# Optimization experiments

Hardware: AMD Instinct MI355X
Metric: run time of the kernel (lower is better)

## Reference

```python
import jax, jax.numpy as jnp
import numpy as np

N, E, IN, OUT, R, B = 20000, 640000, 256, 800, 8, 8


def setup_inputs() -> dict:
    key = jax.random.key(0)
    k0, k1, k2, k3, k4, k5 = jax.random.split(key, 6)
    x = jax.random.normal(k0, (N, IN), dtype=jnp.float32)
    edge_index = jax.random.randint(k1, (2, E), 0, N, dtype=jnp.int32)
    edge_type = jax.random.randint(k2, (E,), 0, R, dtype=jnp.int32)
    # basis-decomposed relation weights: W_r = sum_b att[r,b] * bases[b]
    bases = jax.random.normal(k3, (B, IN, OUT), dtype=jnp.float32) * 0.05
    att = jax.random.normal(k4, (R, B), dtype=jnp.float32) * 0.3
    root = jax.random.normal(k5, (IN, OUT), dtype=jnp.float32) * 0.05
    bias = jnp.zeros((OUT,), dtype=jnp.float32)
    return {"x": x, "edge_index": edge_index, "edge_type": edge_type,
            "bases": bases, "att": att, "root": root, "bias": bias}


def reference(x, edge_index, edge_type, bases, att, root, bias):
    # RGCNConv (basis decomposition, scatter-add aggregation):
    #   out[v] = sum_{(u->v, r) in edges} x[u] @ W_r  +  x[v] @ root  +  bias
    # Efficient form: first segment-sum x[src] per (dst, relation), then one
    # dense contraction with the R relation weights (math-identical for add-aggr).
    n, in_dim = x.shape
    r, b = att.shape
    W = jnp.einsum('rb,bio->rio', att, bases)          # [R, IN, OUT]
    src, dst = edge_index[0], edge_index[1]
    seg = dst.astype(jnp.int32) * r + edge_type.astype(jnp.int32)
    # per-(node, relation) sums of source features: [N*R, IN] -> [N, R, IN]
    s = jax.ops.segment_sum(x[src], seg, num_segments=n * r).reshape(n, r, in_dim)
    out = jnp.einsum('nri,rio->no', s, W) + x @ root + bias
    return out
```

## Files before the change

### kernel.cpp

```cpp
#include <hip/hip_runtime.h>


#define N_NODES 20000
#define N_EDGES 640000
#define IN_DIM  256
#define OUT_DIM 800
#define NREL    8
#define NSEG    160000
#define KS      2048
#define KTOT    2304
#define NPAD    1024
#define NB      625

#define BM 256
#define BN 160
#define BK 64
#define NKT (KTOT / BK)
#define MT  79
#define NT  5
#define NWG (MT * NT)
#define ABYTES 32768
#define LBUF 53248

#define XCAST_B (N_NODES * 64 / 256)
#define WCAT_B  ((KTOT / 8) * 4)
#define INIT_NWG (NB + XCAST_B + WCAT_B)

typedef float f32x4_t __attribute__((ext_vector_type(4)));
typedef short short8_t __attribute__((ext_vector_type(8)));

__device__ __forceinline__ unsigned short f2bf(float f) {
  unsigned u = __float_as_uint(f);
  u += 0x7fffu + ((u >> 16) & 1u);
  return (unsigned short)(u >> 16);
}

__device__ __forceinline__ float bflo(unsigned w) { return __uint_as_float(w << 16); }
__device__ __forceinline__ float bfhi(unsigned w) { return __uint_as_float(w & 0xffff0000u); }

__device__ __forceinline__ void gload16(const void* g, void* l) {
  __builtin_amdgcn_global_load_lds(
      (const __attribute__((address_space(1))) void*)g,
      (__attribute__((address_space(3))) void*)l, 16, 0, 0);
}

__global__ void init_kernel(const float* __restrict__ x,
                            const float* __restrict__ bases,
                            const float* __restrict__ att,
                            const float* __restrict__ root,
                            int* __restrict__ cnt,
                            unsigned short* __restrict__ abf,
                            unsigned short* __restrict__ wcatT) {
  const int b = blockIdx.x;
  const int t = threadIdx.x;
  if (b < NB) {
    cnt[b * 256 + t] = 0;
  } else if (b < NB + XCAST_B) {
    const int id = (b - NB) * 256 + t;
    const int row = id >> 6, lane = id & 63;
    const float4 v = ((const float4*)x)[(size_t)row * 64 + lane];
    union { unsigned short u[4]; uint2 q; } pk;
    pk.u[0] = f2bf(v.x); pk.u[1] = f2bf(v.y);
    pk.u[2] = f2bf(v.z); pk.u[3] = f2bf(v.w);
    *(uint2*)(abf + (size_t)row * KTOT + KS + lane * 4) = pk.q;
  } else {
    const int rem = b - NB - XCAST_B;
    const int kc = rem >> 2, ng = rem & 3;
    const int k0 = kc * 8;
    const int n  = ng * 256 + t;
    if (n >= OUT_DIM) return;
    union { unsigned short u[8]; uint4 q; } pk;
    if (k0 < KS) {
      const int r = k0 >> 8, i0 = k0 & 255;
      float av[8];
      #pragma unroll
      for (int bb = 0; bb < 8; ++bb) av[bb] = att[r * 8 + bb];
      #pragma unroll
      for (int j = 0; j < 8; ++j) {
        float v = 0.f;
        #pragma unroll
        for (int bb = 0; bb < 8; ++bb)
          v += av[bb] * bases[((size_t)bb * IN_DIM + i0 + j) * OUT_DIM + n];
        pk.u[j] = f2bf(v);
      }
    } else {
      #pragma unroll
      for (int j = 0; j < 8; ++j)
        pk.u[j] = f2bf(root[(size_t)(k0 - KS + j) * OUT_DIM + n]);
    }
    *(uint4*)(wcatT + (size_t)n * KTOT + k0) = pk.q;
  }
}


__global__ void hist_kernel(const int* __restrict__ ei, const int* __restrict__ et,
                            int* __restrict__ cnt) {
  const int e = blockIdx.x * 256 + threadIdx.x;
  const int seg = ei[N_EDGES + e] * NREL + et[e];
  atomicAdd(&cnt[seg], 1);
}

__global__ void scan_reduce_kernel(const int* __restrict__ cnt, int* __restrict__ bsum) {
  __shared__ int sm[256];
  const int t = threadIdx.x;
  sm[t] = cnt[blockIdx.x * 256 + t];
  __syncthreads();
  for (int s = 128; s > 0; s >>= 1) {
    if (t < s) sm[t] += sm[t + s];
    __syncthreads();
  }
  if (t == 0) bsum[blockIdx.x] = sm[0];
}

__global__ void scan_bsum_kernel(int* __restrict__ bsum) {
  __shared__ int sm[1024];
  const int t = threadIdx.x;
  const int v = (t < NB) ? bsum[t] : 0;
  sm[t] = v;
  __syncthreads();
  for (int s = 1; s < 1024; s <<= 1) {
    const int a = (t >= s) ? sm[t - s] : 0;
    __syncthreads();
    sm[t] += a;
    __syncthreads();
  }
  if (t < NB) bsum[t] = sm[t] - v;
}

__global__ void scan_final_kernel(const int* __restrict__ cnt, const int* __restrict__ bsum,
                                  int* __restrict__ off, int* __restrict__ cur) {
  __shared__ int sm[256];
  const int t = threadIdx.x;
  const int g = blockIdx.x * 256 + t;
  const int v = cnt[g];
  sm[t] = v;
  __syncthreads();
  for (int s = 1; s < 256; s <<= 1) {
    const int a = (t >= s) ? sm[t - s] : 0;
    __syncthreads();
    sm[t] += a;
    __syncthreads();
  }
  const int ex = sm[t] - v + bsum[blockIdx.x];
  off[g] = ex;
  cur[g] = ex;
}

__global__ void reorder_kernel(const int* __restrict__ ei, const int* __restrict__ et,
                               int* __restrict__ cur, int* __restrict__ sorted_src) {
  const int e = blockIdx.x * 256 + threadIdx.x;
  const int seg = ei[N_EDGES + e] * NREL + et[e];
  const int pos = atomicAdd(&cur[seg], 1);
  sorted_src[pos] = ei[e];
}

__global__ void aggregate_kernel(const int* __restrict__ cnt, const int* __restrict__ off,
                                 const int* __restrict__ sorted_src,
                                 unsigned short* __restrict__ abf) {
  const int seg = __builtin_amdgcn_readfirstlane(blockIdx.x * 4 + (threadIdx.x >> 6));
  const int l = threadIdx.x & 63;
  const int half = l >> 5;
  const int sl = l & 31;
  const int ne = cnt[seg];
  const int o  = off[seg];
  float a0 = 0.f, a1 = 0.f, a2 = 0.f, a3 = 0.f;
  float a4 = 0.f, a5 = 0.f, a6 = 0.f, a7 = 0.f;
  int j = 0;
  for (; j + 2 <= ne; j += 2) {
    const int s = sorted_src[o + j + half];
    const uint4 u = *(const uint4*)(abf + (size_t)s * KTOT + KS + sl * 8);
    a0 += bflo(u.x); a1 += bfhi(u.x); a2 += bflo(u.y); a3 += bfhi(u.y);
    a4 += bflo(u.z); a5 += bfhi(u.z); a6 += bflo(u.w); a7 += bfhi(u.w);
  }
  if (j < ne && half == 0) {
    const int s = sorted_src[o + j];
    const uint4 u = *(const uint4*)(abf + (size_t)s * KTOT + KS + sl * 8);
    a0 += bflo(u.x); a1 += bfhi(u.x); a2 += bflo(u.y); a3 += bfhi(u.y);
    a4 += bflo(u.z); a5 += bfhi(u.z); a6 += bflo(u.w); a7 += bfhi(u.w);
  }
  a0 += __shfl_xor(a0, 32); a1 += __shfl_xor(a1, 32);
  a2 += __shfl_xor(a2, 32); a3 += __shfl_xor(a3, 32);
  a4 += __shfl_xor(a4, 32); a5 += __shfl_xor(a5, 32);
  a6 += __shfl_xor(a6, 32); a7 += __shfl_xor(a7, 32);
  if (half == 0) {
    const int node = seg >> 3, r = seg & 7;
    union { unsigned short u[8]; uint4 q; } pk;
    pk.u[0] = f2bf(a0); pk.u[1] = f2bf(a1); pk.u[2] = f2bf(a2); pk.u[3] = f2bf(a3);
    pk.u[4] = f2bf(a4); pk.u[5] = f2bf(a5); pk.u[6] = f2bf(a6); pk.u[7] = f2bf(a7);
    *(uint4*)(abf + (size_t)node * KTOT + r * IN_DIM + sl * 8) = pk.q;
  }
}

__global__ __launch_bounds__(512) void gemm_kernel(
    const unsigned short* __restrict__ abf,
    const unsigned short* __restrict__ wcatT,
    const float* __restrict__ bias, float* __restrict__ out) {
  __shared__ __align__(16) char lds[3 * LBUF];

  const int lin = blockIdx.x;
  const int q8 = NWG >> 3, r8 = NWG & 7;
  const int xcd = lin & 7, idx = lin >> 3;
  const int wg = (xcd < r8 ? xcd * (q8 + 1) : r8 * (q8 + 1) + (xcd - r8) * q8) + idx;
  const int row0 = (wg / NT) * BM;
  const int col0 = (wg % NT) * BN;

  const int tid = threadIdx.x;
  const int w = tid >> 6, l = tid & 63;
  const int wm = w >> 1, wn = w & 1;
  const int la = l & 15, lg = l >> 4;
  const int l3 = l >> 3;
  const int sch = (l & 7) ^ l3;

  const unsigned short* gA[4];
  #pragma unroll
  for (int i = 0; i < 4; ++i) {
    int ga = row0 + i * 64 + w * 8 + l3;
    ga = (ga < N_NODES) ? ga : (N_NODES - 1);
    gA[i] = abf + (size_t)ga * KTOT + sch * 8;
  }
  const int b2row = (w < 4) ? (128 + w * 8 + l3) : ((w - 4) * 8 + l3);
  const unsigned short* gB0 = wcatT + (size_t)(col0 + w * 8 + l3) * KTOT + sch * 8;
  const unsigned short* gB1 = wcatT + (size_t)(col0 + 64 + w * 8 + l3) * KTOT + sch * 8;
  const unsigned short* gB2 = wcatT + (size_t)(col0 + b2row) * KTOT + sch * 8;
  const int dB2 = (w < 4) ? (ABYTES + 16384 + w * 1024) : (ABYTES + (w - 4) * 1024);

  f32x4_t acc[4][5];
  #pragma unroll
  for (int i = 0; i < 4; ++i)
    #pragma unroll
    for (int j = 0; j < 5; ++j)
      acc[i][j] = (f32x4_t)(0.0f);

  auto stage_all = [&](int buf, int kt) {
    char* base = lds + buf * LBUF;
    const int ko = kt * BK;
    gload16(gA[0] + ko, base + w * 1024);
    gload16(gA[1] + ko, base + 8192 + w * 1024);
    gload16(gA[2] + ko, base + 16384 + w * 1024);
    gload16(gA[3] + ko, base + 24576 + w * 1024);
    gload16(gB0 + ko, base + ABYTES + w * 1024);
    gload16(gB1 + ko, base + ABYTES + 8192 + w * 1024);
    gload16(gB2 + ko, base + dB2);
  };

  stage_all(0, 0);
  stage_all(1, 1);

  for (int kt = 0; kt < NKT; ++kt) {
    const int cbuf = kt % 3;
    const int pbuf = (kt + 2) % 3;
    const bool pf = (kt + 2) < NKT;
    const int pko = (kt + 2) * BK;
    const char* Ab = lds + cbuf * LBUF;
    const char* Bb = Ab + ABYTES;
    char* pbase = lds + pbuf * LBUF;

    if (kt + 1 < NKT) { asm volatile("s_waitcnt vmcnt(7)" ::: "memory"); }
    else              { asm volatile("s_waitcnt vmcnt(0)" ::: "memory"); }
    __builtin_amdgcn_sched_barrier(0);
    __builtin_amdgcn_s_barrier();

    short8_t af0, af1, bfv[5];

    {
      const int r0 = wm * 64 + la, r1 = wm * 64 + 16 + la;
      af0 = *(const short8_t*)(Ab + r0 * 128 + ((lg << 4) ^ ((r0 & 7) << 4)));
      af1 = *(const short8_t*)(Ab + r1 * 128 + ((lg << 4) ^ ((r1 & 7) << 4)));
      #pragma unroll
      for (int nf = 0; nf < 5; ++nf) {
        const int rr = wn * 80 + nf * 16 + la;
        bfv[nf] = *(const short8_t*)(Bb + rr * 128 + ((lg << 4) ^ ((rr & 7) << 4)));
      }
      if (pf) { gload16(gA[0] + pko, pbase + w * 1024);
                gload16(gA[1] + pko, pbase + 8192 + w * 1024); }
      __builtin_amdgcn_s_barrier();
      asm volatile("s_waitcnt lgkmcnt(0)" ::: "memory");
      __builtin_amdgcn_sched_barrier(0);
      __builtin_amdgcn_s_setprio(1);
      #pragma unroll
      for (int nf = 0; nf < 5; ++nf)
        acc[0][nf] = __builtin_amdgcn_mfma_f32_16x16x32_bf16(af0, bfv[nf], acc[0][nf], 0, 0, 0);
      #pragma unroll
      for (int nf = 0; nf < 5; ++nf)
        acc[1][nf] = __builtin_amdgcn_mfma_f32_16x16x32_bf16(af1, bfv[nf], acc[1][nf], 0, 0, 0);
      __builtin_amdgcn_s_setprio(0);
      __builtin_amdgcn_s_barrier();
    }
    {
      const int r0 = wm * 64 + 32 + la, r1 = wm * 64 + 48 + la;
      af0 = *(const short8_t*)(Ab + r0 * 128 + ((lg << 4) ^ ((r0 & 7) << 4)));
      af1 = *(const short8_t*)(Ab + r1 * 128 + ((lg << 4) ^ ((r1 & 7) << 4)));
      if (pf) { gload16(gA[2] + pko, pbase + 16384 + w * 1024);
                gload16(gA[3] + pko, pbase + 24576 + w * 1024); }
      __builtin_amdgcn_s_barrier();
      asm volatile("s_waitcnt lgkmcnt(0)" ::: "memory");
      __builtin_amdgcn_sched_barrier(0);
      __builtin_amdgcn_s_setprio(1);
      #pragma unroll
      for (int nf = 0; nf < 5; ++nf)
        acc[2][nf] = __builtin_amdgcn_mfma_f32_16x16x32_bf16(af0, bfv[nf], acc[2][nf], 0, 0, 0);
      #pragma unroll
      for (int nf = 0; nf < 5; ++nf)
        acc[3][nf] = __builtin_amdgcn_mfma_f32_16x16x32_bf16(af1, bfv[nf], acc[3][nf], 0, 0, 0);
      __builtin_amdgcn_s_setprio(0);
      __builtin_amdgcn_s_barrier();
    }
    {
      const int r0 = wm * 64 + la, r1 = wm * 64 + 16 + la;
      af0 = *(const short8_t*)(Ab + r0 * 128 + (((4 + lg) << 4) ^ ((r0 & 7) << 4)));
      af1 = *(const short8_t*)(Ab + r1 * 128 + (((4 + lg) << 4) ^ ((r1 & 7) << 4)));
      #pragma unroll
      for (int nf = 0; nf < 5; ++nf) {
        const int rr = wn * 80 + nf * 16 + la;
        bfv[nf] = *(const short8_t*)(Bb + rr * 128 + (((4 + lg) << 4) ^ ((rr & 7) << 4)));
      }
      if (pf) { gload16(gB0 + pko, pbase + ABYTES + w * 1024);
                gload16(gB1 + pko, pbase + ABYTES + 8192 + w * 1024); }
      __builtin_amdgcn_s_barrier();
      asm volatile("s_waitcnt lgkmcnt(0)" ::: "memory");
      __builtin_amdgcn_sched_barrier(0);
      __builtin_amdgcn_s_setprio(1);
      #pragma unroll
      for (int nf = 0; nf < 5; ++nf)
        acc[0][nf] = __builtin_amdgcn_mfma_f32_16x16x32_bf16(af0, bfv[nf], acc[0][nf], 0, 0, 0);
      #pragma unroll
      for (int nf = 0; nf < 5; ++nf)
        acc[1][nf] = __builtin_amdgcn_mfma_f32_16x16x32_bf16(af1, bfv[nf], acc[1][nf], 0, 0, 0);
      __builtin_amdgcn_s_setprio(0);
      __builtin_amdgcn_s_barrier();
    }
    {
      const int r0 = wm * 64 + 32 + la, r1 = wm * 64 + 48 + la;
      af0 = *(const short8_t*)(Ab + r0 * 128 + (((4 + lg) << 4) ^ ((r0 & 7) << 4)));
      af1 = *(const short8_t*)(Ab + r1 * 128 + (((4 + lg) << 4) ^ ((r1 & 7) << 4)));
      if (pf) { gload16(gB2 + pko, pbase + dB2); }
      __builtin_amdgcn_s_barrier();
      asm volatile("s_waitcnt lgkmcnt(0)" ::: "memory");
      __builtin_amdgcn_sched_barrier(0);
      __builtin_amdgcn_s_setprio(1);
      #pragma unroll
      for (int nf = 0; nf < 5; ++nf)
        acc[2][nf] = __builtin_amdgcn_mfma_f32_16x16x32_bf16(af0, bfv[nf], acc[2][nf], 0, 0, 0);
      #pragma unroll
      for (int nf = 0; nf < 5; ++nf)
        acc[3][nf] = __builtin_amdgcn_mfma_f32_16x16x32_bf16(af1, bfv[nf], acc[3][nf], 0, 0, 0);
      __builtin_amdgcn_s_setprio(0);
      __builtin_amdgcn_s_barrier();
    }
  }

  #pragma unroll
  for (int nf = 0; nf < 5; ++nf) {
    const int gcol = col0 + wn * 80 + nf * 16 + la;
    const float bv = bias[gcol];
    #pragma unroll
    for (int f = 0; f < 4; ++f) {
      const int gr0 = row0 + wm * 64 + f * 16 + lg * 4;
      #pragma unroll
      for (int j = 0; j < 4; ++j) {
        const int gr = gr0 + j;
        if (gr < N_NODES)
          out[(size_t)gr * OUT_DIM + gcol] = acc[f][nf][j] + bv;
      }
    }
  }
}

extern "C" void kernel_launch(void* const* d_in, const int* in_sizes, int n_in,
                              void* d_out, int out_size, void* d_ws, size_t ws_size,
                              hipStream_t stream) {
  const float* x     = (const float*)d_in[0];
  const int*   ei    = (const int*)d_in[1];
  const int*   et    = (const int*)d_in[2];
  const float* bases = (const float*)d_in[3];
  const float* att   = (const float*)d_in[4];
  const float* root  = (const float*)d_in[5];
  const float* bias  = (const float*)d_in[6];
  float* out = (float*)d_out;

  char* p = (char*)d_ws;
  unsigned short* abf   = (unsigned short*)p;  p += (size_t)N_NODES * KTOT * 2;
  unsigned short* wcatT = (unsigned short*)p;  p += (size_t)NPAD * KTOT * 2;
  int* cnt        = (int*)p;                   p += (size_t)NSEG * 4;
  int* off        = (int*)p;                   p += (size_t)NSEG * 4;
  int* cur        = (int*)p;                   p += (size_t)NSEG * 4;
  int* sorted_src = (int*)p;                   p += (size_t)N_EDGES * 4;
  int* bsum       = (int*)p;                   p += 4096;

  init_kernel<<<INIT_NWG, 256, 0, stream>>>(x, bases, att, root, cnt, abf, wcatT);
  hist_kernel<<<N_EDGES / 256, 256, 0, stream>>>(ei, et, cnt);
  scan_reduce_kernel<<<NB, 256, 0, stream>>>(cnt, bsum);
  scan_bsum_kernel<<<1, 1024, 0, stream>>>(bsum);
  scan_final_kernel<<<NB, 256, 0, stream>>>(cnt, bsum, off, cur);
  reorder_kernel<<<N_EDGES / 256, 256, 0, stream>>>(ei, et, cur, sorted_src);
  aggregate_kernel<<<NSEG / 4, 256, 0, stream>>>(cnt, off, sorted_src, abf);
  gemm_kernel<<<NWG, 512, 0, stream>>>(abf, wcatT, bias, out);
}
```

Baseline: 241.8 us.

## Replace three-pass prefix scan with atomic block allocation; vectorize edge loads

Replaces the global exclusive scan (reduce, block-sum scan, final scan kernels) with a single kernel in which each block scans its 256 counts locally and claims a base offset through one atomicAdd on a global counter. This removes two kernel launches and the serialized single-block scan. Segments end up in arbitrary block order rather than sorted order, but each segment stays contiguous, so aggregation is still correct. The histogram and reorder kernels now handle four edges per thread using int4 loads, which cuts the block count.

```diff
diff --git a/kernel.cpp b/kernel.cpp
--- a/kernel.cpp
+++ b/kernel.cpp
@@ -50,11 +50,13 @@
                             const float* __restrict__ root,
                             int* __restrict__ cnt,
                             unsigned short* __restrict__ abf,
-                            unsigned short* __restrict__ wcatT) {
+                            unsigned short* __restrict__ wcatT,
+                            int* __restrict__ gtotal) {
   const int b = blockIdx.x;
   const int t = threadIdx.x;
   if (b < NB) {
     cnt[b * 256 + t] = 0;
+    if (b == 0 && t == 0) *gtotal = 0;
   } else if (b < NB + XCAST_B) {
     const int id = (b - NB) * 256 + t;
     const int row = id >> 6, lane = id & 63;
@@ -95,41 +97,19 @@
 
 __global__ void hist_kernel(const int* __restrict__ ei, const int* __restrict__ et,
                             int* __restrict__ cnt) {
-  const int e = blockIdx.x * 256 + threadIdx.x;
-  const int seg = ei[N_EDGES + e] * NREL + et[e];
-  atomicAdd(&cnt[seg], 1);
-}
-
-__global__ void scan_reduce_kernel(const int* __restrict__ cnt, int* __restrict__ bsum) {
+  const int e0 = (blockIdx.x * 256 + threadIdx.x) * 4;
+  const int4 d = *(const int4*)(ei + N_EDGES + e0);
+  const int4 r = *(const int4*)(et + e0);
+  atomicAdd(&cnt[d.x * NREL + r.x], 1);
+  atomicAdd(&cnt[d.y * NREL + r.y], 1);
+  atomicAdd(&cnt[d.z * NREL + r.z], 1);
+  atomicAdd(&cnt[d.w * NREL + r.w], 1);
+}
+
+__global__ void alloc_kernel(const int* __restrict__ cnt, int* __restrict__ off,
+                             int* __restrict__ cur, int* __restrict__ gtotal) {
   __shared__ int sm[256];
-  const int t = threadIdx.x;
-  sm[t] = cnt[blockIdx.x * 256 + t];
-  __syncthreads();
-  for (int s = 128; s > 0; s >>= 1) {
-    if (t < s) sm[t] += sm[t + s];
-    __syncthreads();
-  }
-  if (t == 0) bsum[blockIdx.x] = sm[0];
-}
-
-__global__ void scan_bsum_kernel(int* __restrict__ bsum) {
-  __shared__ int sm[1024];
-  const int t = threadIdx.x;
-  const int v = (t < NB) ? bsum[t] : 0;
-  sm[t] = v;
-  __syncthreads();
-  for (int s = 1; s < 1024; s <<= 1) {
-    const int a = (t >= s) ? sm[t - s] : 0;
-    __syncthreads();
-    sm[t] += a;
-    __syncthreads();
-  }
-  if (t < NB) bsum[t] = sm[t] - v;
-}
-
-__global__ void scan_final_kernel(const int* __restrict__ cnt, const int* __restrict__ bsum,
-                                  int* __restrict__ off, int* __restrict__ cur) {
-  __shared__ int sm[256];
+  __shared__ int sbase;
   const int t = threadIdx.x;
   const int g = blockIdx.x * 256 + t;
   const int v = cnt[g];
@@ -141,17 +121,23 @@
     sm[t] += a;
     __syncthreads();
   }
-  const int ex = sm[t] - v + bsum[blockIdx.x];
+  if (t == 255) sbase = atomicAdd(gtotal, sm[255]);
+  __syncthreads();
+  const int ex = sm[t] - v + sbase;
   off[g] = ex;
   cur[g] = ex;
 }
 
 __global__ void reorder_kernel(const int* __restrict__ ei, const int* __restrict__ et,
                                int* __restrict__ cur, int* __restrict__ sorted_src) {
-  const int e = blockIdx.x * 256 + threadIdx.x;
-  const int seg = ei[N_EDGES + e] * NREL + et[e];
-  const int pos = atomicAdd(&cur[seg], 1);
-  sorted_src[pos] = ei[e];
+  const int e0 = (blockIdx.x * 256 + threadIdx.x) * 4;
+  const int4 s = *(const int4*)(ei + e0);
+  const int4 d = *(const int4*)(ei + N_EDGES + e0);
+  const int4 r = *(const int4*)(et + e0);
+  sorted_src[atomicAdd(&cur[d.x * NREL + r.x], 1)] = s.x;
+  sorted_src[atomicAdd(&cur[d.y * NREL + r.y], 1)] = s.y;
+  sorted_src[atomicAdd(&cur[d.z * NREL + r.z], 1)] = s.z;
+  sorted_src[atomicAdd(&cur[d.w * NREL + r.w], 1)] = s.w;
 }
 
 __global__ void aggregate_kernel(const int* __restrict__ cnt, const int* __restrict__ off,
@@ -385,14 +371,12 @@
   int* off        = (int*)p;                   p += (size_t)NSEG * 4;
   int* cur        = (int*)p;                   p += (size_t)NSEG * 4;
   int* sorted_src = (int*)p;                   p += (size_t)N_EDGES * 4;
-  int* bsum       = (int*)p;                   p += 4096;
-
-  init_kernel<<<INIT_NWG, 256, 0, stream>>>(x, bases, att, root, cnt, abf, wcatT);
-  hist_kernel<<<N_EDGES / 256, 256, 0, stream>>>(ei, et, cnt);
-  scan_reduce_kernel<<<NB, 256, 0, stream>>>(cnt, bsum);
-  scan_bsum_kernel<<<1, 1024, 0, stream>>>(bsum);
-  scan_final_kernel<<<NB, 256, 0, stream>>>(cnt, bsum, off, cur);
-  reorder_kernel<<<N_EDGES / 256, 256, 0, stream>>>(ei, et, cur, sorted_src);
+  int* gtotal     = (int*)p;                   p += 4096;
+
+  init_kernel<<<INIT_NWG, 256, 0, stream>>>(x, bases, att, root, cnt, abf, wcatT, gtotal);
+  hist_kernel<<<N_EDGES / 1024, 256, 0, stream>>>(ei, et, cnt);
+  alloc_kernel<<<NB, 256, 0, stream>>>(cnt, off, cur, gtotal);
+  reorder_kernel<<<N_EDGES / 1024, 256, 0, stream>>>(ei, et, cur, sorted_src);
   aggregate_kernel<<<NSEG / 4, 256, 0, stream>>>(cnt, off, sorted_src, abf);
   gemm_kernel<<<NWG, 512, 0, stream>>>(abf, wcatT, bias, out);
 }
```

Result: no change. 242.6 us (+0.3%).
